# Kernel tuning notes

Measured on AMD Instinct MI355X. Metric: run time of the kernel, lower is better.

The kernel has to match this reference:

```python
import jax, jax.numpy as jnp
import numpy as np

EPS = 1e-5

def setup_inputs() -> dict:
    key = jax.random.key(0)
    k1, k2, k3 = jax.random.split(key, 3)
    B, C, V, L, O = 16, 64, 20000, 9, 64
    x = jax.random.normal(k1, (B, C, V), dtype=jnp.float32)
    spiral_idx = jax.random.randint(k2, (V, L), 0, V, dtype=jnp.int32)
    W = jax.random.normal(k3, (O, C * L), dtype=jnp.float32) * 0.02
    b = jnp.zeros((O,), dtype=jnp.float32)
    gamma = jnp.ones((O,), dtype=jnp.float32)
    beta = jnp.zeros((O,), dtype=jnp.float32)
    return {"x": x, "spiral_idx": spiral_idx, "W": W, "b": b, "gamma": gamma, "beta": beta}

def reference(x, spiral_idx, W, b, gamma, beta):
    B, C, V = x.shape
    L = spiral_idx.shape[1]
    # spiral neighbor gather: neigh[b,c,v,l] = x[b,c,spiral_idx[v,l]]  -> [B,C,V,L]
    neigh = x[:, :, spiral_idx]
    # faithful row-major reshape as in the torch module (mixes V and L)
    neigh = neigh.reshape(B, C * L, V)
    # 1x1 Conv1d == matmul over channel dim
    out = jnp.einsum('om,bmv->bov', W, neigh) + b[None, :, None]
    # BatchNorm1d (training mode: biased batch stats over B and V)
    mean = out.mean(axis=(0, 2), keepdims=True)
    var = ((out - mean) ** 2).mean(axis=(0, 2), keepdims=True)
    y = gamma[None, :, None] * (out - mean) * jax.lax.rsqrt(var + EPS) + beta[None, :, None]
    return jnp.maximum(y, 0.0)
```

## Files before the change

### kernel.cpp

```cpp
#include <hip/hip_runtime.h>
#include <hip/hip_bf16.h>
#include <cstdint>
#include <cstddef>

#define B_ 16
#define C_ 64
#define V_ 20000
#define L_ 9
#define O_ 64
#define K_ 576
#define NBV (B_*V_)

typedef short bf16x8 __attribute__((ext_vector_type(8)));
typedef float f32x4  __attribute__((ext_vector_type(4)));

__device__ inline unsigned short f2bf(float f) {
    union { float f; unsigned u; } x; x.f = f;
    unsigned r = (x.u + 0x7fffu + ((x.u >> 16) & 1u)) >> 16;
    return (unsigned short)r;
}

#define BARRIER() do { \
    asm volatile("s_waitcnt lgkmcnt(0)" ::: "memory"); \
    __builtin_amdgcn_s_barrier(); \
} while (0)
#define VMW(N) asm volatile("s_waitcnt vmcnt(" #N ")" ::: "memory")

__global__ __launch_bounds__(256) void k_tx(const float* __restrict__ x,
                                            ushort* __restrict__ xTb) {
    __shared__ float t[C_][33];
    const int b  = blockIdx.y;
    const int v0 = blockIdx.x * 32;
    const int tid = threadIdx.x;
    {
        const int c  = tid >> 2;
        const int jj = tid & 3;
        const float* src = x + ((size_t)b * C_ + c) * V_ + v0 + jj * 8;
        float4 f0 = ((const float4*)src)[0];
        float4 f1 = ((const float4*)src)[1];
        t[c][jj*8+0] = f0.x; t[c][jj*8+1] = f0.y; t[c][jj*8+2] = f0.z; t[c][jj*8+3] = f0.w;
        t[c][jj*8+4] = f1.x; t[c][jj*8+5] = f1.y; t[c][jj*8+6] = f1.z; t[c][jj*8+7] = f1.w;
    }
    __syncthreads();
    {
        const int vl = tid & 31;
        const int cg = tid >> 5;
        union { ushort u[8]; uint4 v4; } pk;
#pragma unroll
        for (int i = 0; i < 8; ++i) pk.u[i] = f2bf(t[cg*8 + i][vl]);
        *(uint4*)(xTb + ((size_t)(b * V_ + v0 + vl)) * 64 + cg * 8) = pk.v4;
    }
}

__global__ __launch_bounds__(256) void k_tw(const float* __restrict__ W,
                                            ushort* __restrict__ Wtb) {
    int gid = blockIdx.x * 256 + threadIdx.x;
    if (gid >= O_ * K_) return;
    int o = gid / K_, kp = gid % K_;
    int tt = kp >> 6, c = kp & 63;
    Wtb[gid] = f2bf(W[o * K_ + c * L_ + tt]);
}

template<bool BF16Y>
__global__ __launch_bounds__(512, 4) void k_conv(const ushort* __restrict__ xTb,
                                                 const int*    __restrict__ S,
                                                 const ushort* __restrict__ Wtb,
                                                 const float*  __restrict__ bias,
                                                 float*  __restrict__ out,
                                                 ushort* __restrict__ yb,
                                                 float* __restrict__ ps,
                                                 float* __restrict__ pq) {
    __shared__ char lds[45056];
    char* nbA = lds;            char* wbA = lds + 16384;
    char* nbB = lds + 20480;    char* wbB = lds + 36864;
    float* sA = (float*)(lds + 40960);
    float* sQ = (float*)(lds + 43008);

    const int tid = threadIdx.x;
    const int v0  = blockIdx.x * 16;
    const int srow = tid >> 1;
    const int h    = tid & 1;
    const int sb   = srow >> 4;
    const int sv   = v0 + (srow & 15);
    const int swzn = (srow >> 1) & 3;
    const int wso  = tid >> 3;
    const int wsl  = tid & 7;
    const int swzo = (wso >> 1) & 3;
    const int w = tid >> 6;
    const int l = tid & 63;
    const int q = l >> 4;
    const int r = l & 15;
    const int fswz = (r >> 1) & 3;

    int gt[L_];
#pragma unroll
    for (int t = 0; t < L_; ++t) gt[t] = S[t * V_ + sv];

    f32x4 acc[2][4];
#pragma unroll
    for (int nt = 0; nt < 2; ++nt)
#pragma unroll
        for (int ot = 0; ot < 4; ++ot) acc[nt][ot] = (f32x4){0.f, 0.f, 0.f, 0.f};

    uint4 rn[2][4];
    uint2 rwv[2][2];

    auto LD = [&](int i, int set) {
        const uint4* p = (const uint4*)(xTb + ((size_t)sb * V_ + gt[i]) * 64 + h * 16);
        rn[set][0] = p[0]; rn[set][1] = p[1];
        rn[set][2] = p[4]; rn[set][3] = p[5];
        const uint2* wp = (const uint2*)(Wtb + (size_t)wso * K_ + i * 64 + wsl * 4);
        rwv[set][0] = wp[0];
        rwv[set][1] = wp[8];
    };
    auto WRN = [&](char* nb, uint4 a, uint4 b2) {
        char* base = nb + srow * 64;
        *(uint4*)(base + ((( 2*h   ) ^ swzn) << 4)) = a;
        *(uint4*)(base + (((2*h + 1) ^ swzn) << 4)) = b2;
    };
    auto WRW = [&](char* wb, uint2 a) {
        const int pos16 = (wsl >> 1) ^ swzo;
        *(uint2*)(wb + wso * 64 + (pos16 << 4) + ((wsl & 1) << 3)) = a;
    };
    auto MM = [&](const char* nb, const char* wb) {
        bf16x8 a0 = *(const bf16x8*)(nb + (w*32      + r) * 64 + ((q ^ fswz) << 4));
        bf16x8 a1 = *(const bf16x8*)(nb + (w*32 + 16 + r) * 64 + ((q ^ fswz) << 4));
#pragma unroll
        for (int ot = 0; ot < 4; ++ot) {
            bf16x8 bo = *(const bf16x8*)(wb + (ot*16 + r) * 64 + ((q ^ fswz) << 4));
            acc[0][ot] = __builtin_amdgcn_mfma_f32_16x16x32_bf16(a0, bo, acc[0][ot], 0, 0, 0);
            acc[1][ot] = __builtin_amdgcn_mfma_f32_16x16x32_bf16(a1, bo, acc[1][ot], 0, 0, 0);
        }
    };

    LD(0, 0);
    LD(1, 1);

#define CONV_ITER(I, VMN)                                                    \
    {                                                                        \
        constexpr int set = (I) & 1;                                         \
        VMW(VMN);                       \
        WRN(nbA, rn[set][0], rn[set][1]); WRW(wbA, rwv[set][0]);             \
        BARRIER();                                                           \
        MM(nbA, wbA);                                                        \
        WRN(nbB, rn[set][2], rn[set][3]); WRW(wbB, rwv[set][1]);             \
        if ((I) < 7) LD((I) + 2, set);                 \
        BARRIER();                                                           \
        MM(nbB, wbB);                                                        \
    }

    CONV_ITER(0, 6)
    CONV_ITER(1, 6)
    CONV_ITER(2, 6)
    CONV_ITER(3, 6)
    CONV_ITER(4, 6)
    CONV_ITER(5, 6)
    CONV_ITER(6, 6)
    CONV_ITER(7, 6)
    CONV_ITER(8, 0)
#undef CONV_ITER

    const int vbase = v0 + q * 4;
    float ssum[4] = {0.f, 0.f, 0.f, 0.f};
    float qsum[4] = {0.f, 0.f, 0.f, 0.f};
#pragma unroll
    for (int ot = 0; ot < 4; ++ot) {
        const int o = ot * 16 + r;
        const float bo = bias[o];
#pragma unroll
        for (int nt = 0; nt < 2; ++nt) {
            const int b = 2 * w + nt;
            float4 y;
            y.x = acc[nt][ot][0] + bo;
            y.y = acc[nt][ot][1] + bo;
            y.z = acc[nt][ot][2] + bo;
            y.w = acc[nt][ot][3] + bo;
            if (BF16Y) {
                ushort4 u;
                u.x = f2bf(y.x); u.y = f2bf(y.y); u.z = f2bf(y.z); u.w = f2bf(y.w);
                *(ushort4*)(yb + ((size_t)(b * O_ + o)) * V_ + vbase) = u;
            } else {
                *(float4*)(out + ((size_t)(b * O_ + o)) * V_ + vbase) = y;
            }
            ssum[ot] += y.x + y.y + y.z + y.w;
            qsum[ot] += y.x*y.x + y.y*y.y + y.z*y.z + y.w*y.w;
        }
    }
#pragma unroll
    for (int ot = 0; ot < 4; ++ot) {
        float s  = ssum[ot], qq = qsum[ot];
        s  += __shfl_xor(s, 16);  s  += __shfl_xor(s, 32);
        qq += __shfl_xor(qq, 16); qq += __shfl_xor(qq, 32);
        if (l < 16) { sA[(ot*16 + l) * 8 + w] = s; sQ[(ot*16 + l) * 8 + w] = qq; }
    }
    __syncthreads();
    if (tid < 64) {
        float s = 0.f, qq = 0.f;
#pragma unroll
        for (int j = 0; j < 8; ++j) { s += sA[tid*8 + j]; qq += sQ[tid*8 + j]; }
        ps[blockIdx.x * 64 + tid] = s;
        pq[blockIdx.x * 64 + tid] = qq;
    }
}

__global__ __launch_bounds__(256) void k_fin(const float* __restrict__ ps,
                                             const float* __restrict__ pq,
                                             const float* __restrict__ gamma,
                                             const float* __restrict__ beta,
                                             float* __restrict__ ss) {
    __shared__ float as_[4], aq_[4];
    const int o = blockIdx.x, tid = threadIdx.x;
    float s = 0.f, q = 0.f;
    for (int i = tid; i < 1250; i += 256) { s += ps[i*64 + o]; q += pq[i*64 + o]; }
#pragma unroll
    for (int off = 1; off < 64; off <<= 1) { s += __shfl_xor(s, off); q += __shfl_xor(q, off); }
    if ((tid & 63) == 0) { as_[tid >> 6] = s; aq_[tid >> 6] = q; }
    __syncthreads();
    if (tid == 0) {
        float S4 = as_[0] + as_[1] + as_[2] + as_[3];
        float Q4 = aq_[0] + aq_[1] + aq_[2] + aq_[3];
        const float n = 1.f / (float)NBV;
        float mean = S4 * n;
        float var  = fmaxf(Q4 * n - mean * mean, 0.f);
        float sc   = gamma[o] * rsqrtf(var + 1e-5f);
        ss[o]      = sc;
        ss[O_ + o] = beta[o] - mean * sc;
    }
}

__global__ __launch_bounds__(256) void k_norm_bf(const ushort* __restrict__ yb,
                                                 float* __restrict__ out,
                                                 const float* __restrict__ ss) {
    const int stride = gridDim.x * blockDim.x;
    const int total8 = (B_ * O_ * V_) / 8;
    for (int i = blockIdx.x * blockDim.x + threadIdx.x; i < total8; i += stride) {
        uint4 raw = ((const uint4*)yb)[i];
        const int row = (i * 8) / V_;
        const int o   = row & 63;
        const float sc = ss[o], sh = ss[O_ + o];
        const uint u32[4] = {raw.x, raw.y, raw.z, raw.w};
        float4 o0, o1;
        float vals[8];
#pragma unroll
        for (int j = 0; j < 4; ++j) {
            union { uint u; float f; } lo, hi;
            lo.u = (u32[j] & 0xffffu) << 16;
            hi.u = (u32[j] & 0xffff0000u);
            vals[2*j]   = lo.f;
            vals[2*j+1] = hi.f;
        }
        o0.x = fmaxf(fmaf(vals[0], sc, sh), 0.f);
        o0.y = fmaxf(fmaf(vals[1], sc, sh), 0.f);
        o0.z = fmaxf(fmaf(vals[2], sc, sh), 0.f);
        o0.w = fmaxf(fmaf(vals[3], sc, sh), 0.f);
        o1.x = fmaxf(fmaf(vals[4], sc, sh), 0.f);
        o1.y = fmaxf(fmaf(vals[5], sc, sh), 0.f);
        o1.z = fmaxf(fmaf(vals[6], sc, sh), 0.f);
        o1.w = fmaxf(fmaf(vals[7], sc, sh), 0.f);
        ((float4*)out)[2*i]   = o0;
        ((float4*)out)[2*i+1] = o1;
    }
}

__global__ __launch_bounds__(256) void k_norm_f32(float* __restrict__ out,
                                                  const float* __restrict__ ss) {
    const int stride = gridDim.x * blockDim.x;
    const int total4 = (B_ * O_ * V_) / 4;
    for (int i = blockIdx.x * blockDim.x + threadIdx.x; i < total4; i += stride) {
        float4 v4 = ((const float4*)out)[i];
        const int row = (i * 4) / V_;
        const int o   = row & 63;
        const float sc = ss[o], sh = ss[O_ + o];
        v4.x = fmaxf(fmaf(v4.x, sc, sh), 0.f);
        v4.y = fmaxf(fmaf(v4.y, sc, sh), 0.f);
        v4.z = fmaxf(fmaf(v4.z, sc, sh), 0.f);
        v4.w = fmaxf(fmaf(v4.w, sc, sh), 0.f);
        ((float4*)out)[i] = v4;
    }
}

extern "C" void kernel_launch(void* const* d_in, const int* in_sizes, int n_in,
                              void* d_out, int out_size, void* d_ws, size_t ws_size,
                              hipStream_t stream) {
    const float* x     = (const float*)d_in[0];
    const int*   S     = (const int*)  d_in[1];
    const float* W     = (const float*)d_in[2];
    const float* bias  = (const float*)d_in[3];
    const float* gamma = (const float*)d_in[4];
    const float* beta  = (const float*)d_in[5];
    float* out = (float*)d_out;

    char* ws = (char*)d_ws;
    const size_t xT_b = 40960000;
    const size_t wt_b = 73728;
    const size_t yb_b = 40960000;
    const size_t ps_b = 320000;

    ushort* xTb = (ushort*)(ws);
    ushort* Wtb = (ushort*)(ws + xT_b);
    const bool bf16y = ws_size >= xT_b + wt_b + yb_b + 2 * ps_b + 512;

    ushort* yb; float* ps; float* pq; float* ssb;
    if (bf16y) {
        yb  = (ushort*)(ws + xT_b + wt_b);
        ps  = (float*) (ws + xT_b + wt_b + yb_b);
        pq  = (float*) (ws + xT_b + wt_b + yb_b + ps_b);
        ssb = (float*) (ws + xT_b + wt_b + yb_b + 2 * ps_b);
    } else {
        yb  = nullptr;
        ps  = (float*) (ws + xT_b + wt_b);
        pq  = (float*) (ws + xT_b + wt_b + ps_b);
        ssb = (float*) (ws + xT_b + wt_b + 2 * ps_b);
    }

    k_tw<<<dim3((O_ * K_ + 255) / 256), dim3(256), 0, stream>>>(W, Wtb);
    k_tx<<<dim3(625, 16),               dim3(256), 0, stream>>>(x, xTb);
    if (bf16y) {
        k_conv<true ><<<dim3(V_ / 16), dim3(512), 0, stream>>>(xTb, S, Wtb, bias, out, yb, ps, pq);
        k_fin<<<dim3(64), dim3(256), 0, stream>>>(ps, pq, gamma, beta, ssb);
        k_norm_bf<<<dim3(2048), dim3(256), 0, stream>>>(yb, out, ssb);
    } else {
        k_conv<false><<<dim3(V_ / 16), dim3(512), 0, stream>>>(xTb, S, Wtb, bias, out, yb, ps, pq);
        k_fin<<<dim3(64), dim3(256), 0, stream>>>(ps, pq, gamma, beta, ssb);
        k_norm_f32<<<dim3(2048), dim3(256), 0, stream>>>(out, ssb);
    }
}
```

Measured before the change: 116.8 us.

## Store transposed x vertex-major across batch and loop conv over tiles persistently

The transposed bf16 copy of x is now laid out as [V][B][C], so all 16 batch rows for one gathered vertex sit in one contiguous 2 KB block. The gather load is remapped so each vertex index is fetched once per tile and its batch rows are read contiguously, which should improve cache-line use and locality for the random spiral gather. The conv kernel also becomes a grid-stride loop over 625 blocks, each handling two tiles, with an extra barrier between tiles. The loop reduces the number of blocks but adds serialization inside each block.

```diff
diff --git a/kernel.cpp b/kernel.cpp
--- a/kernel.cpp
+++ b/kernel.cpp
@@ -48,7 +48,7 @@
         union { ushort u[8]; uint4 v4; } pk;
 #pragma unroll
         for (int i = 0; i < 8; ++i) pk.u[i] = f2bf(t[cg*8 + i][vl]);
-        *(uint4*)(xTb + ((size_t)(b * V_ + v0 + vl)) * 64 + cg * 8) = pk.v4;
+        *(uint4*)(xTb + ((size_t)(v0 + vl) * B_ + b) * 64 + cg * 8) = pk.v4;
     }
 }
 
@@ -77,12 +77,12 @@
     float* sQ = (float*)(lds + 43008);
 
     const int tid = threadIdx.x;
-    const int v0  = blockIdx.x * 16;
-    const int srow = tid >> 1;
-    const int h    = tid & 1;
-    const int sb   = srow >> 4;
-    const int sv   = v0 + (srow & 15);
-    const int swzn = (srow >> 1) & 3;
+    const int vr   = tid >> 5;
+    const int sbb  = (tid & 31) >> 1;
+    const int part = tid & 1;
+    const int nrow = sbb * 16 + vr;
+    const int boff = sbb * 128 + part * 32;
+    const int swzn = (vr >> 1) & 3;
     const int wso  = tid >> 3;
     const int wsl  = tid & 7;
     const int swzo = (wso >> 1) & 3;
@@ -92,114 +92,121 @@
     const int r = l & 15;
     const int fswz = (r >> 1) & 3;
 
-    int gt[L_];
-#pragma unroll
-    for (int t = 0; t < L_; ++t) gt[t] = S[t * V_ + sv];
-
-    f32x4 acc[2][4];
-#pragma unroll
-    for (int nt = 0; nt < 2; ++nt)
-#pragma unroll
-        for (int ot = 0; ot < 4; ++ot) acc[nt][ot] = (f32x4){0.f, 0.f, 0.f, 0.f};
-
-    uint4 rn[2][4];
-    uint2 rwv[2][2];
-
-    auto LD = [&](int i, int set) {
-        const uint4* p = (const uint4*)(xTb + ((size_t)sb * V_ + gt[i]) * 64 + h * 16);
-        rn[set][0] = p[0]; rn[set][1] = p[1];
-        rn[set][2] = p[4]; rn[set][3] = p[5];
-        const uint2* wp = (const uint2*)(Wtb + (size_t)wso * K_ + i * 64 + wsl * 4);
-        rwv[set][0] = wp[0];
-        rwv[set][1] = wp[8];
-    };
-    auto WRN = [&](char* nb, uint4 a, uint4 b2) {
-        char* base = nb + srow * 64;
-        *(uint4*)(base + ((( 2*h   ) ^ swzn) << 4)) = a;
-        *(uint4*)(base + (((2*h + 1) ^ swzn) << 4)) = b2;
-    };
-    auto WRW = [&](char* wb, uint2 a) {
-        const int pos16 = (wsl >> 1) ^ swzo;
-        *(uint2*)(wb + wso * 64 + (pos16 << 4) + ((wsl & 1) << 3)) = a;
-    };
-    auto MM = [&](const char* nb, const char* wb) {
-        bf16x8 a0 = *(const bf16x8*)(nb + (w*32      + r) * 64 + ((q ^ fswz) << 4));
-        bf16x8 a1 = *(const bf16x8*)(nb + (w*32 + 16 + r) * 64 + ((q ^ fswz) << 4));
+    for (int tile = blockIdx.x; tile < V_ / 16; tile += gridDim.x) {
+        const int v0 = tile * 16;
+
+        int gtv[L_];
+#pragma unroll
+        for (int t = 0; t < L_; ++t) gtv[t] = S[t * V_ + v0 + vr];
+
+        f32x4 acc[2][4];
+#pragma unroll
+        for (int nt = 0; nt < 2; ++nt)
+#pragma unroll
+            for (int ot = 0; ot < 4; ++ot) acc[nt][ot] = (f32x4){0.f, 0.f, 0.f, 0.f};
+
+        uint4 rn[2][4];
+        uint2 rwv[2][2];
+
+        auto LD = [&](int i, int set) {
+            const char* rowp = (const char*)xTb + (size_t)gtv[i] * 2048 + boff;
+            rn[set][0] = *(const uint4*)(rowp);
+            rn[set][1] = *(const uint4*)(rowp + 16);
+            rn[set][2] = *(const uint4*)(rowp + 64);
+            rn[set][3] = *(const uint4*)(rowp + 80);
+            const uint2* wp = (const uint2*)(Wtb + (size_t)wso * K_ + i * 64 + wsl * 4);
+            rwv[set][0] = wp[0];
+            rwv[set][1] = wp[8];
+        };
+        auto WRN = [&](char* nb, uint4 a, uint4 b2) {
+            char* base = nb + nrow * 64;
+            *(uint4*)(base + (((part*2    ) ^ swzn) << 4)) = a;
+            *(uint4*)(base + (((part*2 + 1) ^ swzn) << 4)) = b2;
+        };
+        auto WRW = [&](char* wb, uint2 a) {
+            const int pos16 = (wsl >> 1) ^ swzo;
+            *(uint2*)(wb + wso * 64 + (pos16 << 4) + ((wsl & 1) << 3)) = a;
+        };
+        auto MM = [&](const char* nb, const char* wb) {
+            bf16x8 a0 = *(const bf16x8*)(nb + (w*32      + r) * 64 + ((q ^ fswz) << 4));
+            bf16x8 a1 = *(const bf16x8*)(nb + (w*32 + 16 + r) * 64 + ((q ^ fswz) << 4));
+#pragma unroll
+            for (int ot = 0; ot < 4; ++ot) {
+                bf16x8 bo = *(const bf16x8*)(wb + (ot*16 + r) * 64 + ((q ^ fswz) << 4));
+                acc[0][ot] = __builtin_amdgcn_mfma_f32_16x16x32_bf16(a0, bo, acc[0][ot], 0, 0, 0);
+                acc[1][ot] = __builtin_amdgcn_mfma_f32_16x16x32_bf16(a1, bo, acc[1][ot], 0, 0, 0);
+            }
+        };
+
+        LD(0, 0);
+        LD(1, 1);
+
+#define CONV_ITER(I, VMN)                                                    \
+        {                                                                    \
+            constexpr int set = (I) & 1;                                     \
+            VMW(VMN);                   \
+            WRN(nbA, rn[set][0], rn[set][1]); WRW(wbA, rwv[set][0]);         \
+            BARRIER();                                                       \
+            MM(nbA, wbA);                                                    \
+            WRN(nbB, rn[set][2], rn[set][3]); WRW(wbB, rwv[set][1]);         \
+            if ((I) < 7) LD((I) + 2, set);             \
+            BARRIER();                                                       \
+            MM(nbB, wbB);                                                    \
+        }
+
+        CONV_ITER(0, 6)
+        CONV_ITER(1, 6)
+        CONV_ITER(2, 6)
+        CONV_ITER(3, 6)
+        CONV_ITER(4, 6)
+        CONV_ITER(5, 6)
+        CONV_ITER(6, 6)
+        CONV_ITER(7, 6)
+        CONV_ITER(8, 0)
+#undef CONV_ITER
+
+        const int vbase = v0 + q * 4;
+        float ssum[4] = {0.f, 0.f, 0.f, 0.f};
+        float qsum[4] = {0.f, 0.f, 0.f, 0.f};
 #pragma unroll
         for (int ot = 0; ot < 4; ++ot) {
-            bf16x8 bo = *(const bf16x8*)(wb + (ot*16 + r) * 64 + ((q ^ fswz) << 4));
-            acc[0][ot] = __builtin_amdgcn_mfma_f32_16x16x32_bf16(a0, bo, acc[0][ot], 0, 0, 0);
-            acc[1][ot] = __builtin_amdgcn_mfma_f32_16x16x32_bf16(a1, bo, acc[1][ot], 0, 0, 0);
-        }
-    };
-
-    LD(0, 0);
-    LD(1, 1);
-
-#define CONV_ITER(I, VMN)                                                    \
-    {                                                                        \
-        constexpr int set = (I) & 1;                                         \
-        VMW(VMN);                       \
-        WRN(nbA, rn[set][0], rn[set][1]); WRW(wbA, rwv[set][0]);             \
-        BARRIER();                                                           \
-        MM(nbA, wbA);                                                        \
-        WRN(nbB, rn[set][2], rn[set][3]); WRW(wbB, rwv[set][1]);             \
-        if ((I) < 7) LD((I) + 2, set);                 \
-        BARRIER();                                                           \
-        MM(nbB, wbB);                                                        \
-    }
-
-    CONV_ITER(0, 6)
-    CONV_ITER(1, 6)
-    CONV_ITER(2, 6)
-    CONV_ITER(3, 6)
-    CONV_ITER(4, 6)
-    CONV_ITER(5, 6)
-    CONV_ITER(6, 6)
-    CONV_ITER(7, 6)
-    CONV_ITER(8, 0)
-#undef CONV_ITER
-
-    const int vbase = v0 + q * 4;
-    float ssum[4] = {0.f, 0.f, 0.f, 0.f};
-    float qsum[4] = {0.f, 0.f, 0.f, 0.f};
-#pragma unroll
-    for (int ot = 0; ot < 4; ++ot) {
-        const int o = ot * 16 + r;
-        const float bo = bias[o];
-#pragma unroll
-        for (int nt = 0; nt < 2; ++nt) {
-            const int b = 2 * w + nt;
-            float4 y;
-            y.x = acc[nt][ot][0] + bo;
-            y.y = acc[nt][ot][1] + bo;
-            y.z = acc[nt][ot][2] + bo;
-            y.w = acc[nt][ot][3] + bo;
-            if (BF16Y) {
-                ushort4 u;
-                u.x = f2bf(y.x); u.y = f2bf(y.y); u.z = f2bf(y.z); u.w = f2bf(y.w);
-                *(ushort4*)(yb + ((size_t)(b * O_ + o)) * V_ + vbase) = u;
-            } else {
-                *(float4*)(out + ((size_t)(b * O_ + o)) * V_ + vbase) = y;
+            const int o = ot * 16 + r;
+            const float bo = bias[o];
+#pragma unroll
+            for (int nt = 0; nt < 2; ++nt) {
+                const int b = 2 * w + nt;
+                float4 y;
+                y.x = acc[nt][ot][0] + bo;
+                y.y = acc[nt][ot][1] + bo;
+                y.z = acc[nt][ot][2] + bo;
+                y.w = acc[nt][ot][3] + bo;
+                if (BF16Y) {
+                    ushort4 u;
+                    u.x = f2bf(y.x); u.y = f2bf(y.y); u.z = f2bf(y.z); u.w = f2bf(y.w);
+                    *(ushort4*)(yb + ((size_t)(b * O_ + o)) * V_ + vbase) = u;
+                } else {
+                    *(float4*)(out + ((size_t)(b * O_ + o)) * V_ + vbase) = y;
+                }
+                ssum[ot] += y.x + y.y + y.z + y.w;
+                qsum[ot] += y.x*y.x + y.y*y.y + y.z*y.z + y.w*y.w;
             }
-            ssum[ot] += y.x + y.y + y.z + y.w;
-            qsum[ot] += y.x*y.x + y.y*y.y + y.z*y.z + y.w*y.w;
-        }
-    }
-#pragma unroll
-    for (int ot = 0; ot < 4; ++ot) {
-        float s  = ssum[ot], qq = qsum[ot];
-        s  += __shfl_xor(s, 16);  s  += __shfl_xor(s, 32);
-        qq += __shfl_xor(qq, 16); qq += __shfl_xor(qq, 32);
-        if (l < 16) { sA[(ot*16 + l) * 8 + w] = s; sQ[(ot*16 + l) * 8 + w] = qq; }
-    }
-    __syncthreads();
-    if (tid < 64) {
-        float s = 0.f, qq = 0.f;
-#pragma unroll
-        for (int j = 0; j < 8; ++j) { s += sA[tid*8 + j]; qq += sQ[tid*8 + j]; }
-        ps[blockIdx.x * 64 + tid] = s;
-        pq[blockIdx.x * 64 + tid] = qq;
+        }
+#pragma unroll
+        for (int ot = 0; ot < 4; ++ot) {
+            float s  = ssum[ot], qq = qsum[ot];
+            s  += __shfl_xor(s, 16);  s  += __shfl_xor(s, 32);
+            qq += __shfl_xor(qq, 16); qq += __shfl_xor(qq, 32);
+            if (l < 16) { sA[(ot*16 + l) * 8 + w] = s; sQ[(ot*16 + l) * 8 + w] = qq; }
+        }
+        __syncthreads();
+        if (tid < 64) {
+            float s = 0.f, qq = 0.f;
+#pragma unroll
+            for (int j = 0; j < 8; ++j) { s += sA[tid*8 + j]; qq += sQ[tid*8 + j]; }
+            ps[tile * 64 + tid] = s;
+            pq[tile * 64 + tid] = qq;
+        }
+        __syncthreads();
     }
 }
 
@@ -316,11 +323,11 @@
     k_tw<<<dim3((O_ * K_ + 255) / 256), dim3(256), 0, stream>>>(W, Wtb);
     k_tx<<<dim3(625, 16),               dim3(256), 0, stream>>>(x, xTb);
     if (bf16y) {
-        k_conv<true ><<<dim3(V_ / 16), dim3(512), 0, stream>>>(xTb, S, Wtb, bias, out, yb, ps, pq);
+        k_conv<true ><<<dim3(625), dim3(512), 0, stream>>>(xTb, S, Wtb, bias, out, yb, ps, pq);
         k_fin<<<dim3(64), dim3(256), 0, stream>>>(ps, pq, gamma, beta, ssb);
         k_norm_bf<<<dim3(2048), dim3(256), 0, stream>>>(yb, out, ssb);
     } else {
-        k_conv<false><<<dim3(V_ / 16), dim3(512), 0, stream>>>(xTb, S, Wtb, bias, out, yb, ps, pq);
+        k_conv<false><<<dim3(625), dim3(512), 0, stream>>>(xTb, S, Wtb, bias, out, yb, ps, pq);
         k_fin<<<dim3(64), dim3(256), 0, stream>>>(ps, pq, gamma, beta, ssb);
         k_norm_f32<<<dim3(2048), dim3(256), 0, stream>>>(out, ssb);
     }
```

After: 134.9 us. 15.5% more time.

## Retile spiral conv per batch with 128-vertex tiles and 256-thread blocks

Applied to the files above, without the earlier changes.

The conv kernel is retiled so each block handles one batch and 128 consecutive vertices, instead of all 16 batches for 16 vertices. Gathers now read one batch slab, which should improve L2 locality across the 8 batches that share an XCD-interleaved block ordering. Blocks shrink to 256 threads with less LDS, and weight loads widen to 16-byte accesses. The price is more blocks and partial-sum rows, bounds checks on the tail tile, and each block re-reading the full weight tile and spiral indices.

```diff
diff --git a/kernel.cpp b/kernel.cpp
--- a/kernel.cpp
+++ b/kernel.cpp
@@ -10,6 +10,8 @@
 #define O_ 64
 #define K_ 576
 #define NBV (B_*V_)
+#define TPB 157
+#define NBLK (TPB*16)
 
 typedef short bf16x8 __attribute__((ext_vector_type(8)));
 typedef float f32x4  __attribute__((ext_vector_type(4)));
@@ -62,7 +64,7 @@
 }
 
 template<bool BF16Y>
-__global__ __launch_bounds__(512, 4) void k_conv(const ushort* __restrict__ xTb,
+__global__ __launch_bounds__(256, 4) void k_conv(const ushort* __restrict__ xTb,
                                                  const int*    __restrict__ S,
                                                  const ushort* __restrict__ Wtb,
                                                  const float*  __restrict__ bias,
@@ -70,21 +72,27 @@
                                                  ushort* __restrict__ yb,
                                                  float* __restrict__ ps,
                                                  float* __restrict__ pq) {
-    __shared__ char lds[45056];
-    char* nbA = lds;            char* wbA = lds + 16384;
-    char* nbB = lds + 20480;    char* wbB = lds + 36864;
-    float* sA = (float*)(lds + 40960);
-    float* sQ = (float*)(lds + 43008);
+    __shared__ char lds[24576];
+    char* nbA = lds;
+    char* wbA = lds + 8192;
+    char* nbB = lds + 12288;
+    char* wbB = lds + 20480;
+    float* sA = (float*)(lds + 8192);
+    float* sQ = (float*)(lds + 9216);
+
+    const int bid  = blockIdx.x;
+    const int half = (bid >= TPB * 8) ? 1 : 0;
+    const int rem  = bid - half * (TPB * 8);
+    const int b    = (rem & 7) | (half << 3);
+    const int vt   = rem >> 3;
+    const int v0   = vt * 128;
 
     const int tid = threadIdx.x;
-    const int v0  = blockIdx.x * 16;
     const int srow = tid >> 1;
     const int h    = tid & 1;
-    const int sb   = srow >> 4;
-    const int sv   = v0 + (srow & 15);
     const int swzn = (srow >> 1) & 3;
-    const int wso  = tid >> 3;
-    const int wsl  = tid & 7;
+    const int wso  = tid >> 2;
+    const int wsl  = tid & 3;
     const int swzo = (wso >> 1) & 3;
     const int w = tid >> 6;
     const int l = tid & 63;
@@ -92,9 +100,13 @@
     const int r = l & 15;
     const int fswz = (r >> 1) & 3;
 
-    int gt[L_];
-#pragma unroll
-    for (int t = 0; t < L_; ++t) gt[t] = S[t * V_ + sv];
+    const int sv  = v0 + srow;
+    const int svc = sv < V_ ? sv : V_ - 1;
+    int gtv[L_];
+#pragma unroll
+    for (int t = 0; t < L_; ++t) gtv[t] = S[t * V_ + svc];
+
+    const size_t slab = (size_t)b * V_;
 
     f32x4 acc[2][4];
 #pragma unroll
@@ -103,24 +115,25 @@
         for (int ot = 0; ot < 4; ++ot) acc[nt][ot] = (f32x4){0.f, 0.f, 0.f, 0.f};
 
     uint4 rn[2][4];
-    uint2 rwv[2][2];
+    uint4 rwq[2][2];
 
     auto LD = [&](int i, int set) {
-        const uint4* p = (const uint4*)(xTb + ((size_t)sb * V_ + gt[i]) * 64 + h * 16);
-        rn[set][0] = p[0]; rn[set][1] = p[1];
-        rn[set][2] = p[4]; rn[set][3] = p[5];
-        const uint2* wp = (const uint2*)(Wtb + (size_t)wso * K_ + i * 64 + wsl * 4);
-        rwv[set][0] = wp[0];
-        rwv[set][1] = wp[8];
+        const char* rowp = (const char*)(xTb + (slab + gtv[i]) * 64) + h * 32;
+        rn[set][0] = *(const uint4*)(rowp);
+        rn[set][1] = *(const uint4*)(rowp + 16);
+        rn[set][2] = *(const uint4*)(rowp + 64);
+        rn[set][3] = *(const uint4*)(rowp + 80);
+        const ushort* wp = Wtb + (size_t)wso * K_ + i * 64 + wsl * 8;
+        rwq[set][0] = *(const uint4*)(wp);
+        rwq[set][1] = *(const uint4*)(wp + 32);
     };
     auto WRN = [&](char* nb, uint4 a, uint4 b2) {
         char* base = nb + srow * 64;
         *(uint4*)(base + ((( 2*h   ) ^ swzn) << 4)) = a;
         *(uint4*)(base + (((2*h + 1) ^ swzn) << 4)) = b2;
     };
-    auto WRW = [&](char* wb, uint2 a) {
-        const int pos16 = (wsl >> 1) ^ swzo;
-        *(uint2*)(wb + wso * 64 + (pos16 << 4) + ((wsl & 1) << 3)) = a;
+    auto WRW = [&](char* wb, uint4 a) {
+        *(uint4*)(wb + wso * 64 + ((wsl ^ swzo) << 4)) = a;
     };
     auto MM = [&](const char* nb, const char* wb) {
         bf16x8 a0 = *(const bf16x8*)(nb + (w*32      + r) * 64 + ((q ^ fswz) << 4));
@@ -140,10 +153,10 @@
     {                                                                        \
         constexpr int set = (I) & 1;                                         \
         VMW(VMN);                       \
-        WRN(nbA, rn[set][0], rn[set][1]); WRW(wbA, rwv[set][0]);             \
+        WRN(nbA, rn[set][0], rn[set][1]); WRW(wbA, rwq[set][0]);             \
         BARRIER();                                                           \
         MM(nbA, wbA);                                                        \
-        WRN(nbB, rn[set][2], rn[set][3]); WRW(wbB, rwv[set][1]);             \
+        WRN(nbB, rn[set][2], rn[set][3]); WRW(wbB, rwq[set][1]);             \
         if ((I) < 7) LD((I) + 2, set);                 \
         BARRIER();                                                           \
         MM(nbB, wbB);                                                        \
@@ -160,7 +173,6 @@
     CONV_ITER(8, 0)
 #undef CONV_ITER
 
-    const int vbase = v0 + q * 4;
     float ssum[4] = {0.f, 0.f, 0.f, 0.f};
     float qsum[4] = {0.f, 0.f, 0.f, 0.f};
 #pragma unroll
@@ -169,21 +181,23 @@
         const float bo = bias[o];
 #pragma unroll
         for (int nt = 0; nt < 2; ++nt) {
-            const int b = 2 * w + nt;
-            float4 y;
-            y.x = acc[nt][ot][0] + bo;
-            y.y = acc[nt][ot][1] + bo;
-            y.z = acc[nt][ot][2] + bo;
-            y.w = acc[nt][ot][3] + bo;
-            if (BF16Y) {
-                ushort4 u;
-                u.x = f2bf(y.x); u.y = f2bf(y.y); u.z = f2bf(y.z); u.w = f2bf(y.w);
-                *(ushort4*)(yb + ((size_t)(b * O_ + o)) * V_ + vbase) = u;
-            } else {
-                *(float4*)(out + ((size_t)(b * O_ + o)) * V_ + vbase) = y;
+            const int v = v0 + w * 32 + nt * 16 + q * 4;
+            if (v < V_) {
+                float4 y;
+                y.x = acc[nt][ot][0] + bo;
+                y.y = acc[nt][ot][1] + bo;
+                y.z = acc[nt][ot][2] + bo;
+                y.w = acc[nt][ot][3] + bo;
+                if (BF16Y) {
+                    ushort4 u;
+                    u.x = f2bf(y.x); u.y = f2bf(y.y); u.z = f2bf(y.z); u.w = f2bf(y.w);
+                    *(ushort4*)(yb + ((size_t)(b * O_ + o)) * V_ + v) = u;
+                } else {
+                    *(float4*)(out + ((size_t)(b * O_ + o)) * V_ + v) = y;
+                }
+                ssum[ot] += y.x + y.y + y.z + y.w;
+                qsum[ot] += y.x*y.x + y.y*y.y + y.z*y.z + y.w*y.w;
             }
-            ssum[ot] += y.x + y.y + y.z + y.w;
-            qsum[ot] += y.x*y.x + y.y*y.y + y.z*y.z + y.w*y.w;
         }
     }
 #pragma unroll
@@ -191,15 +205,15 @@
         float s  = ssum[ot], qq = qsum[ot];
         s  += __shfl_xor(s, 16);  s  += __shfl_xor(s, 32);
         qq += __shfl_xor(qq, 16); qq += __shfl_xor(qq, 32);
-        if (l < 16) { sA[(ot*16 + l) * 8 + w] = s; sQ[(ot*16 + l) * 8 + w] = qq; }
+        if (l < 16) { sA[(ot*16 + l) * 4 + w] = s; sQ[(ot*16 + l) * 4 + w] = qq; }
     }
     __syncthreads();
     if (tid < 64) {
         float s = 0.f, qq = 0.f;
 #pragma unroll
-        for (int j = 0; j < 8; ++j) { s += sA[tid*8 + j]; qq += sQ[tid*8 + j]; }
-        ps[blockIdx.x * 64 + tid] = s;
-        pq[blockIdx.x * 64 + tid] = qq;
+        for (int j = 0; j < 4; ++j) { s += sA[tid*4 + j]; qq += sQ[tid*4 + j]; }
+        ps[bid * 64 + tid] = s;
+        pq[bid * 64 + tid] = qq;
     }
 }
 
@@ -211,7 +225,7 @@
     __shared__ float as_[4], aq_[4];
     const int o = blockIdx.x, tid = threadIdx.x;
     float s = 0.f, q = 0.f;
-    for (int i = tid; i < 1250; i += 256) { s += ps[i*64 + o]; q += pq[i*64 + o]; }
+    for (int i = tid; i < NBLK; i += 256) { s += ps[i*64 + o]; q += pq[i*64 + o]; }
 #pragma unroll
     for (int off = 1; off < 64; off <<= 1) { s += __shfl_xor(s, off); q += __shfl_xor(q, off); }
     if ((tid & 63) == 0) { as_[tid >> 6] = s; aq_[tid >> 6] = q; }
@@ -294,7 +308,7 @@
     const size_t xT_b = 40960000;
     const size_t wt_b = 73728;
     const size_t yb_b = 40960000;
-    const size_t ps_b = 320000;
+    const size_t ps_b = (size_t)NBLK * 64 * 4;
 
     ushort* xTb = (ushort*)(ws);
     ushort* Wtb = (ushort*)(ws + xT_b);
@@ -316,11 +330,11 @@
     k_tw<<<dim3((O_ * K_ + 255) / 256), dim3(256), 0, stream>>>(W, Wtb);
     k_tx<<<dim3(625, 16),               dim3(256), 0, stream>>>(x, xTb);
     if (bf16y) {
-        k_conv<true ><<<dim3(V_ / 16), dim3(512), 0, stream>>>(xTb, S, Wtb, bias, out, yb, ps, pq);
+        k_conv<true ><<<dim3(NBLK), dim3(256), 0, stream>>>(xTb, S, Wtb, bias, out, yb, ps, pq);
         k_fin<<<dim3(64), dim3(256), 0, stream>>>(ps, pq, gamma, beta, ssb);
         k_norm_bf<<<dim3(2048), dim3(256), 0, stream>>>(yb, out, ssb);
     } else {
-        k_conv<false><<<dim3(V_ / 16), dim3(512), 0, stream>>>(xTb, S, Wtb, bias, out, yb, ps, pq);
+        k_conv<false><<<dim3(NBLK), dim3(256), 0, stream>>>(xTb, S, Wtb, bias, out, yb, ps, pq);
         k_fin<<<dim3(64), dim3(256), 0, stream>>>(ps, pq, gamma, beta, ssb);
         k_norm_f32<<<dim3(2048), dim3(256), 0, stream>>>(out, ssb);
     }
```

After: 99.90 us. 1.17x faster.
